# Performance work log

Measured on AMD Instinct MI355X. Metric: run time of the kernel, lower is better.

The kernel has to match this reference:

```python
import jax, jax.numpy as jnp
import numpy as np

C = 16          # n_tasks (channels) = num_tasks - 1
NUM_TASKS = 17  # IndexKernel size
RANK = 3        # IndexKernel rank (hard-coded in source)
JITTER = 1e-4
N_MC = 10
N_CLASSES = 10

def _rbf(x1, x2, ls):
    d = (x1[:, None] - x2[None, :]) / ls
    return jnp.exp(-0.5 * d * d)

def _gp_posterior(x, i_tr, y, xs, i_te, c, ls, noise, Btask):
    # Exact GP posterior with Hadamard multitask kernel k(x,x')*B[i,i'].
    T = x.shape[0]
    Kxx = _rbf(x, x, ls) * Btask[i_tr][:, i_tr] + (noise * noise + JITTER) * jnp.eye(T, dtype=x.dtype)
    Ksx = _rbf(xs, x, ls) * Btask[i_te][:, i_tr]
    Kss = _rbf(xs, xs, ls) * Btask[i_te][:, i_te]
    L = jnp.linalg.cholesky(Kxx)
    alpha = jax.scipy.linalg.cho_solve((L, True), y - c)
    mean = c + Ksx @ alpha
    V = jax.scipy.linalg.solve_triangular(L, Ksx.T, lower=True)  # [T, Ts]
    cov = Kss - V.T @ V
    return mean, cov

def _channel_reshape(Z_raw, test_idx):
    # Vectorized version of the triple-loop ragged scatter.
    # Z_raw: [S, B, Ts]; test_idx: [B, Ts] int -> Z: [S, B, max_len, C]
    S, Bb, Ts = Z_raw.shape
    max_len = Ts // C
    onehot = jax.nn.one_hot(test_idx, C, dtype=jnp.int32)                       # [B, Ts, C]
    before = jnp.cumsum(onehot, axis=1) - onehot                                # same-channel count before elem
    pos = jnp.take_along_axis(before, test_idx[..., None], axis=-1)[..., 0]     # [B, Ts]
    b_idx = jnp.broadcast_to(jnp.arange(Bb)[:, None], (Bb, Ts))
    Z = jnp.zeros((S, Bb, max_len, C), Z_raw.dtype)
    return Z.at[:, b_idx, pos, test_idx].set(Z_raw)

def setup_inputs() -> dict:
    key = jax.random.key(0)
    ks = jax.random.split(key, 8)
    B, T, Ts = 32, 1024, 1024
    inputs = jax.random.uniform(ks[0], (B, T, 1), jnp.float32) * 10.0
    indices = jax.random.randint(ks[1], (B, T, 1), 0, C)
    values = jax.random.normal(ks[2], (B, T), jnp.float32)
    test_inputs = jax.random.uniform(ks[3], (B, Ts, 1), jnp.float32) * 10.0
    test_indices = (jnp.arange(Ts, dtype=jnp.int32)[None, :, None] % C) * jnp.ones((B, 1, 1), jnp.int32)
    eps = jax.random.normal(ks[4], (N_MC, B, Ts), jnp.float32)
    mean_const = jnp.zeros((), jnp.float32)
    lengthscale = jnp.ones((), jnp.float32)
    noise = 0.3 * jnp.ones((), jnp.float32)
    W_task = jax.random.normal(ks[5], (NUM_TASKS, RANK), jnp.float32) * 0.3
    v_task = jax.random.uniform(ks[6], (NUM_TASKS,), jnp.float32)
    W_clf = jax.random.normal(ks[7], (C, N_CLASSES), jnp.float32) * 0.1
    b_clf = jnp.zeros((N_CLASSES,), jnp.float32)
    return dict(inputs=inputs, values=values, test_inputs=test_inputs, eps=eps,
                mean_const=mean_const, lengthscale=lengthscale, noise=noise,
                W_task=W_task, v_task=v_task, W_clf=W_clf, b_clf=b_clf,
                indices=indices, test_indices=test_indices)

def reference(inputs, values, test_inputs, eps, mean_const, lengthscale, noise,
              W_task, v_task, W_clf, b_clf, indices, test_indices):
    Btask = W_task @ W_task.T + jnp.diag(jax.nn.softplus(v_task))  # IndexKernel: B = W W^T + diag(v)
    x, xs = inputs[..., 0], test_inputs[..., 0]
    i_tr, i_te = indices[..., 0], test_indices[..., 0]
    mean, cov = jax.vmap(_gp_posterior, in_axes=(0, 0, 0, 0, 0, None, None, None, None))(
        x, i_tr, values, xs, i_te, mean_const, lengthscale, noise, Btask)
    Ts = xs.shape[1]
    Lstar = jnp.linalg.cholesky(cov + JITTER * jnp.eye(Ts, dtype=cov.dtype))
    samples = mean[None] + jnp.einsum('bij,sbj->sbi', Lstar, eps)   # rsample: [S, B, Ts]
    Z = _channel_reshape(samples, i_te)                              # [S, B, max_len, C]
    S, Bb, ml, _ = Z.shape
    Zc = Z.reshape(S * Bb, ml, C)                                    # monte_carlo collapse (flatten(0,1))
    feat = Zc.mean(axis=1)                                           # clf: mean pool + linear
    return feat @ W_clf + b_clf
```

## Files before the change

### kernel.cpp

```cpp
#include <hip/hip_runtime.h>
#include <math.h>

#define TT 1024
#define CH 16
#define SMC 10
#define NCLS 10
#define JIT 1e-4f

__device__ __forceinline__ void tri_map(int tau, int& ti, int& tj) {
    int i = 0, r = tau;
    while (r >= i + 1) { r -= i + 1; i++; }
    ti = i; tj = r;
}

__global__ __launch_bounds__(256) void k_btask(const float* __restrict__ W,
                                               const float* __restrict__ v,
                                               float* __restrict__ Bt) {
    int t = threadIdx.x;
    for (int e = t; e < 17 * 17; e += 256) {
        int i = e / 17, j = e % 17;
        float s = 0.f;
        for (int r = 0; r < 3; r++) s += W[i * 3 + r] * W[j * 3 + r];
        if (i == j) s += log1pf(expf(v[i]));
        Bt[e] = s;
    }
}

__global__ __launch_bounds__(256) void k_build_kxx(const float* __restrict__ x,
                                                   const int* __restrict__ itr,
                                                   const float* __restrict__ lsp,
                                                   const float* __restrict__ noisep,
                                                   const float* __restrict__ Bt,
                                                   float* __restrict__ A, int b0) {
    int bi = blockIdx.x, bj = blockIdx.y, bz = blockIdx.z;
    if (bj > bi) return;
    int b = b0 + bz;
    __shared__ float sxi[128], sxj[128], Btl[289];
    __shared__ int sii[128], sij[128];
    int t = threadIdx.x;
    if (t < 128) { sxi[t] = x[b * TT + bi * 128 + t]; sii[t] = itr[b * TT + bi * 128 + t]; }
    else { int u = t - 128; sxj[u] = x[b * TT + bj * 128 + u]; sij[u] = itr[b * TT + bj * 128 + u]; }
    for (int e = t; e < 289; e += 256) Btl[e] = Bt[e];
    __syncthreads();
    float invls = 1.0f / lsp[0];
    float n2 = noisep[0] * noisep[0] + JIT;
    float* Ab = A + (size_t)bz * TT * TT;
    for (int l = 0; l < 64; l++) {
        int e = l * 256 + t;
        int r = e >> 7, c = e & 127;
        float d = (sxi[r] - sxj[c]) * invls;
        float kv = expf(-0.5f * d * d) * Btl[sii[r] * 17 + sij[c]];
        int gi = bi * 128 + r, gj = bj * 128 + c;
        if (gi == gj) kv += n2;
        Ab[(size_t)gi * TT + gj] = kv;
    }
}

__global__ __launch_bounds__(256) void k_build_g(const float* __restrict__ xs,
                                                 const float* __restrict__ x,
                                                 const int* __restrict__ ite,
                                                 const int* __restrict__ itr,
                                                 const float* __restrict__ lsp,
                                                 const float* __restrict__ Bt,
                                                 float* __restrict__ G, int b0) {
    int bj = blockIdx.x, bi = blockIdx.y, bz = blockIdx.z;
    int b = b0 + bz;
    __shared__ float sxr[128], sxc[128], Btl[289];
    __shared__ int sir[128], sic[128];
    int t = threadIdx.x;
    if (t < 128) { sxr[t] = x[b * TT + bj * 128 + t]; sir[t] = itr[b * TT + bj * 128 + t]; }
    else { int u = t - 128; sxc[u] = xs[b * TT + bi * 128 + u]; sic[u] = ite[b * TT + bi * 128 + u]; }
    for (int e = t; e < 289; e += 256) Btl[e] = Bt[e];
    __syncthreads();
    float invls = 1.0f / lsp[0];
    float* Gb = G + (size_t)bz * TT * TT;
    for (int l = 0; l < 64; l++) {
        int e = l * 256 + t;
        int r = e >> 7, c = e & 127;
        float d = (sxc[c] - sxr[r]) * invls;
        float kv = expf(-0.5f * d * d) * Btl[sic[c] * 17 + sir[r]];
        Gb[(size_t)(bj * 128 + r) * TT + bi * 128 + c] = kv;
    }
}

__global__ __launch_bounds__(256) void k_zinit(const float* __restrict__ values,
                                               const float* __restrict__ mc,
                                               float* __restrict__ zb, int b0) {
    int bz = blockIdx.x, t = threadIdx.x;
    float c0 = mc[0];
    for (int i = t; i < TT; i += 256) zb[bz * TT + i] = values[(size_t)(b0 + bz) * TT + i] - c0;
}

__global__ __launch_bounds__(256) void k_stepA64(float* __restrict__ A,
                                                 float* __restrict__ G,
                                                 float* __restrict__ zb,
                                                 float* __restrict__ Dfac,
                                                 int k, int m, int withG) {
    int bx = blockIdx.x, bz = blockIdx.y;
    float* Ab = A + (size_t)bz * TT * TT;
    float* Gb = G + (size_t)bz * TT * TT;
    int kb = k * 64;
    __shared__ float Ld[64][65];
    __shared__ float WK[64][129];
    __shared__ float invl[64];
    __shared__ float zs[64];
    int t = threadIdx.x;
    for (int l = 0; l < 16; l++) {
        int e = l * 256 + t; int r = e >> 6, c = e & 63;
        Ld[r][c] = Ab[(size_t)(kb + r) * TT + kb + c];
    }
    int jtype = 0, r0 = 0, c0 = 0;
    if (bx >= 1 && bx <= m) {
        jtype = 1; r0 = kb + 64 * bx;
        for (int l = 0; l < 16; l++) {
            int e = l * 256 + t; int r = e >> 6, c = e & 63;
            WK[r][c] = Ab[(size_t)(r0 + r) * TT + kb + c];
        }
    } else if (withG && bx >= m + 1 && bx <= m + 8) {
        jtype = 2; c0 = (bx - m - 1) * 128;
        for (int l = 0; l < 32; l++) {
            int e = l * 256 + t; int r = e >> 7, c = e & 127;
            WK[r][c] = Gb[(size_t)(kb + r) * TT + c0 + c];
        }
    } else if (withG && bx == m + 9) {
        jtype = 3;
        if (t < 64) zs[t] = zb[bz * TT + kb + t];
    }
    __syncthreads();
    for (int j = 0; j < 64; j++) {
        if (t == j) { float d = sqrtf(Ld[j][j]); Ld[j][j] = d; invl[j] = 1.0f / d; }
        __syncthreads();
        float lij = 0.f;
        if (t < 64 && t > j) { lij = Ld[t][j] * invl[j]; Ld[t][j] = lij; }
        __syncthreads();
        if (t < 64 && t > j) {
#pragma unroll 4
            for (int p = j + 1; p <= t; p++) Ld[t][p] -= lij * Ld[p][j];
        }
    }
    __syncthreads();
    if (jtype == 0) {
        if (bx == 0) {
            float* Df = Dfac + ((size_t)bz * 16 + k) * 4096;
            for (int l = 0; l < 16; l++) {
                int e = l * 256 + t; int r = e >> 6, c = e & 63;
                Df[r * 64 + c] = Ld[r][c];
            }
        }
        return;
    }
    if (jtype == 1) {
        if (t < 64) {
            for (int j = 0; j < 64; j++) {
                float xv = WK[t][j] * invl[j];
                WK[t][j] = xv;
#pragma unroll 4
                for (int p = j + 1; p < 64; p++) WK[t][p] -= Ld[p][j] * xv;
            }
        }
        __syncthreads();
        for (int l = 0; l < 16; l++) {
            int e = l * 256 + t; int r = e >> 6, c = e & 63;
            Ab[(size_t)(r0 + r) * TT + kb + c] = WK[r][c];
        }
    } else if (jtype == 2) {
        if (t < 128) {
            for (int j = 0; j < 64; j++) {
                float xv = WK[j][t] * invl[j];
                WK[j][t] = xv;
#pragma unroll 4
                for (int p = j + 1; p < 64; p++) WK[p][t] -= Ld[p][j] * xv;
            }
        }
        __syncthreads();
        for (int l = 0; l < 32; l++) {
            int e = l * 256 + t; int r = e >> 7, c = e & 127;
            Gb[(size_t)(kb + r) * TT + c0 + c] = WK[r][c];
        }
    } else {
        if (t == 0) {
            for (int j = 0; j < 64; j++) {
                float zv = zs[j] * invl[j];
                zs[j] = zv;
#pragma unroll 4
                for (int p = j + 1; p < 64; p++) zs[p] -= Ld[p][j] * zv;
            }
        }
        __syncthreads();
        if (t < 64) zb[bz * TT + kb + t] = zs[t];
    }
}

__global__ __launch_bounds__(256) void k_diagfix64(float* __restrict__ A,
                                                   const float* __restrict__ Dfac) {
    int k = blockIdx.x, bz = blockIdx.y;
    int kb = k * 64;
    float* Ab = A + (size_t)bz * TT * TT;
    const float* Df = Dfac + ((size_t)bz * 16 + k) * 4096;
    int t = threadIdx.x;
    for (int l = 0; l < 16; l++) {
        int e = l * 256 + t; int r = e >> 6, c = e & 63;
        if (c <= r) Ab[(size_t)(kb + r) * TT + kb + c] = Df[r * 64 + c];
    }
}

__global__ __launch_bounds__(256) void k_stepB64(float* __restrict__ A,
                                                 float* __restrict__ G,
                                                 float* __restrict__ zb,
                                                 int k, int m, int bc, int withG) {
    int lin = blockIdx.x;
    int slot = lin & 7, q = lin >> 3;
    int beta = ((slot - 4 * (q & 1)) & 7) + (blockIdx.y << 3);
    if (beta >= bc) return;
    float* Ab = A + (size_t)beta * TT * TT;
    float* Gb = G + (size_t)beta * TT * TT;
    int kb = k * 64;
    int nt = (64 * m + 127) / 128;
    int TL = nt * (nt + 1) / 2;
    __shared__ __align__(16) float At[32][132];
    __shared__ __align__(16) float Bs[32][132];
    __shared__ float zk[64];
    int t = threadIdx.x, tx = t & 15, ty = t >> 4;
    if (q < TL) {
        int ti, tj; tri_map(q, ti, tj);
        int base = kb + 64;
        int r0 = base + ti * 128, c0 = base + tj * 128;
        int rvi = TT - r0; if (rvi > 128) rvi = 128;
        int rvj = TT - c0; if (rvj > 128) rvj = 128;
        float acc[8][8] = {};
        for (int s = 0; s < 2; s++) {
            int k0 = kb + s * 32;
            __syncthreads();
            for (int l = 0; l < 4; l++) {
                int f = l * 256 + t;
                int r = f >> 3, c4 = (f & 7) * 4;
                float4 va = make_float4(0.f, 0.f, 0.f, 0.f), vb = make_float4(0.f, 0.f, 0.f, 0.f);
                if (r < rvi) va = *reinterpret_cast<const float4*>(&Ab[(size_t)(r0 + r) * TT + k0 + c4]);
                if (r < rvj) vb = *reinterpret_cast<const float4*>(&Ab[(size_t)(c0 + r) * TT + k0 + c4]);
                At[c4 + 0][r] = va.x; At[c4 + 1][r] = va.y; At[c4 + 2][r] = va.z; At[c4 + 3][r] = va.w;
                Bs[c4 + 0][r] = vb.x; Bs[c4 + 1][r] = vb.y; Bs[c4 + 2][r] = vb.z; Bs[c4 + 3][r] = vb.w;
            }
            __syncthreads();
#pragma unroll 4
            for (int p = 0; p < 32; p++) {
                float4 a0 = *reinterpret_cast<const float4*>(&At[p][ty * 8]);
                float4 a1 = *reinterpret_cast<const float4*>(&At[p][ty * 8 + 4]);
                float4 b0 = *reinterpret_cast<const float4*>(&Bs[p][tx * 4]);
                float4 b1 = *reinterpret_cast<const float4*>(&Bs[p][tx * 4 + 64]);
                float aa[8] = {a0.x, a0.y, a0.z, a0.w, a1.x, a1.y, a1.z, a1.w};
                float bl[4] = {b0.x, b0.y, b0.z, b0.w};
                float bh[4] = {b1.x, b1.y, b1.z, b1.w};
                for (int i = 0; i < 8; i++) {
                    for (int j = 0; j < 4; j++) acc[i][j] += aa[i] * bl[j];
                    for (int j = 0; j < 4; j++) acc[i][j + 4] += aa[i] * bh[j];
                }
            }
        }
        if (tx * 4 >= rvj) return;
        for (int i = 0; i < 8; i++) {
            int rr = ty * 8 + i;
            if (rr >= rvi) break;
            float* cp0 = &Ab[(size_t)(r0 + rr) * TT + c0 + tx * 4];
            float4 cv0 = *reinterpret_cast<float4*>(cp0);
            cv0.x -= acc[i][0]; cv0.y -= acc[i][1]; cv0.z -= acc[i][2]; cv0.w -= acc[i][3];
            *reinterpret_cast<float4*>(cp0) = cv0;
            if (rvj > 64) {
                float* cp1 = cp0 + 64;
                float4 cv1 = *reinterpret_cast<float4*>(cp1);
                cv1.x -= acc[i][4]; cv1.y -= acc[i][5]; cv1.z -= acc[i][6]; cv1.w -= acc[i][7];
                *reinterpret_cast<float4*>(cp1) = cv1;
            }
        }
        return;
    }
    int e = q - TL;
    int ti = e / 9, sub = e % 9;
    int r0 = kb + 64 + ti * 128;
    int rvi = TT - r0; if (rvi > 128) rvi = 128;
    if (sub < 8) {
        int c0 = sub * 128;
        float acc[8][8] = {};
        for (int s = 0; s < 2; s++) {
            int k0 = kb + s * 32;
            __syncthreads();
            for (int l = 0; l < 4; l++) {
                int f = l * 256 + t;
                int r = f >> 3, c4 = (f & 7) * 4;
                float4 va = make_float4(0.f, 0.f, 0.f, 0.f);
                if (r < rvi) va = *reinterpret_cast<const float4*>(&Ab[(size_t)(r0 + r) * TT + k0 + c4]);
                At[c4 + 0][r] = va.x; At[c4 + 1][r] = va.y; At[c4 + 2][r] = va.z; At[c4 + 3][r] = va.w;
                int kr = f >> 5, cc4 = (f & 31) * 4;
                float4 vb = *reinterpret_cast<const float4*>(&Gb[(size_t)(k0 + kr) * TT + c0 + cc4]);
                *reinterpret_cast<float4*>(&Bs[kr][cc4]) = vb;
            }
            __syncthreads();
#pragma unroll 4
            for (int p = 0; p < 32; p++) {
                float4 a0 = *reinterpret_cast<const float4*>(&At[p][ty * 8]);
                float4 a1 = *reinterpret_cast<const float4*>(&At[p][ty * 8 + 4]);
                float4 b0 = *reinterpret_cast<const float4*>(&Bs[p][tx * 4]);
                float4 b1 = *reinterpret_cast<const float4*>(&Bs[p][tx * 4 + 64]);
                float aa[8] = {a0.x, a0.y, a0.z, a0.w, a1.x, a1.y, a1.z, a1.w};
                float bl[4] = {b0.x, b0.y, b0.z, b0.w};
                float bh[4] = {b1.x, b1.y, b1.z, b1.w};
                for (int i = 0; i < 8; i++) {
                    for (int j = 0; j < 4; j++) acc[i][j] += aa[i] * bl[j];
                    for (int j = 0; j < 4; j++) acc[i][j + 4] += aa[i] * bh[j];
                }
            }
        }
        for (int i = 0; i < 8; i++) {
            int rr = ty * 8 + i;
            if (rr >= rvi) break;
            float* cp0 = &Gb[(size_t)(r0 + rr) * TT + c0 + tx * 4];
            float4 cv0 = *reinterpret_cast<float4*>(cp0);
            cv0.x -= acc[i][0]; cv0.y -= acc[i][1]; cv0.z -= acc[i][2]; cv0.w -= acc[i][3];
            *reinterpret_cast<float4*>(cp0) = cv0;
            float* cp1 = cp0 + 64;
            float4 cv1 = *reinterpret_cast<float4*>(cp1);
            cv1.x -= acc[i][4]; cv1.y -= acc[i][5]; cv1.z -= acc[i][6]; cv1.w -= acc[i][7];
            *reinterpret_cast<float4*>(cp1) = cv1;
        }
    } else {
        if (t < 64) zk[t] = zb[beta * TT + kb + t];
        float accz = 0.f;
        for (int s = 0; s < 2; s++) {
            int k0 = kb + s * 32;
            __syncthreads();
            for (int l = 0; l < 4; l++) {
                int f = l * 256 + t;
                int r = f >> 3, c4 = (f & 7) * 4;
                float4 va = make_float4(0.f, 0.f, 0.f, 0.f);
                if (r < rvi) va = *reinterpret_cast<const float4*>(&Ab[(size_t)(r0 + r) * TT + k0 + c4]);
                At[c4 + 0][r] = va.x; At[c4 + 1][r] = va.y; At[c4 + 2][r] = va.z; At[c4 + 3][r] = va.w;
            }
            __syncthreads();
            if (t < 128) {
                for (int qq = 0; qq < 32; qq++) accz += At[qq][t] * zk[s * 32 + qq];
            }
        }
        if (t < rvi) zb[beta * TT + r0 + t] -= accz;
    }
}

__global__ __launch_bounds__(256) void k_cov64(const float* __restrict__ G,
                                               const float* __restrict__ xs,
                                               const int* __restrict__ ite,
                                               const float* __restrict__ lsp,
                                               const float* __restrict__ Bt,
                                               float* __restrict__ A,
                                               const float* __restrict__ zb,
                                               const float* __restrict__ mc,
                                               float* __restrict__ meanb,
                                               int b0, int bc) {
    int lin = blockIdx.x;
    int slot = lin & 7, tau = lin >> 3;
    int beta = ((slot - 4 * (tau & 1)) & 7) + (blockIdx.y << 3);
    if (beta >= bc) return;
    int ti, tj; tri_map(tau, ti, tj);
    int b = b0 + beta;
    const float* Gb = G + (size_t)beta * TT * TT;
    float* Ab = A + (size_t)beta * TT * TT;
    int i0 = ti * 64, j0 = tj * 64;
    __shared__ __align__(16) float Va[32][68];
    __shared__ __align__(16) float Vb[32][68];
    __shared__ float sxi[64], sxj[64], Btl[289], zs[32];
    __shared__ int sei[64], sej[64];
    int t = threadIdx.x, tx = t & 15, ty = t >> 4;
    if (t < 64) { sxi[t] = xs[b * TT + i0 + t]; sei[t] = ite[b * TT + i0 + t]; }
    else if (t < 128) { int u = t - 64; sxj[u] = xs[b * TT + j0 + u]; sej[u] = ite[b * TT + j0 + u]; }
    for (int e = t; e < 289; e += 256) Btl[e] = Bt[e];
    bool diag = (ti == tj);
    float acc[4][4] = {};
    float macc[4] = {0.f, 0.f, 0.f, 0.f};
    for (int k0 = 0; k0 < TT; k0 += 32) {
        __syncthreads();
        for (int l = 0; l < 2; l++) {
            int f = l * 256 + t;
            int kr = f >> 4, cc4 = (f & 15) * 4;
            *reinterpret_cast<float4*>(&Va[kr][cc4]) =
                *reinterpret_cast<const float4*>(&Gb[(size_t)(k0 + kr) * TT + i0 + cc4]);
            *reinterpret_cast<float4*>(&Vb[kr][cc4]) =
                *reinterpret_cast<const float4*>(&Gb[(size_t)(k0 + kr) * TT + j0 + cc4]);
        }
        if (diag && t < 32) zs[t] = zb[beta * TT + k0 + t];
        __syncthreads();
#pragma unroll 4
        for (int p = 0; p < 32; p++) {
            float4 av = *reinterpret_cast<const float4*>(&Va[p][ty * 4]);
            float4 bv = *reinterpret_cast<const float4*>(&Vb[p][tx * 4]);
            float aa[4] = {av.x, av.y, av.z, av.w};
            float bb[4] = {bv.x, bv.y, bv.z, bv.w};
            for (int i = 0; i < 4; i++)
                for (int j = 0; j < 4; j++) acc[i][j] += aa[i] * bb[j];
        }
        if (diag && ty == 0) {
#pragma unroll 4
            for (int p = 0; p < 32; p++) {
                float zv = zs[p];
                float4 av = *reinterpret_cast<const float4*>(&Va[p][tx * 4]);
                macc[0] += av.x * zv; macc[1] += av.y * zv;
                macc[2] += av.z * zv; macc[3] += av.w * zv;
            }
        }
    }
    float invls = 1.0f / lsp[0];
    for (int i = 0; i < 4; i++) {
        int ri = ty * 4 + i; int gi = i0 + ri;
        float xi = sxi[ri]; int ci = sei[ri] * 17;
        float vo[4];
        for (int j = 0; j < 4; j++) {
            int rj = tx * 4 + j; int gj = j0 + rj;
            float d = (xi - sxj[rj]) * invls;
            float v = expf(-0.5f * d * d) * Btl[ci + sej[rj]] - acc[i][j];
            if (gi == gj) v += JIT;
            vo[j] = v;
        }
        *reinterpret_cast<float4*>(&Ab[(size_t)gi * TT + j0 + tx * 4]) =
            make_float4(vo[0], vo[1], vo[2], vo[3]);
    }
    if (diag && ty == 0) {
        float c0 = mc[0];
        for (int j = 0; j < 4; j++)
            meanb[(size_t)b * TT + i0 + tx * 4 + j] = c0 + macc[j];
    }
}

__global__ __launch_bounds__(256) void k_P(const float* __restrict__ A,
                                           const int* __restrict__ ite,
                                           float* __restrict__ P, int b0) {
    int bz = blockIdx.y; int b = b0 + bz;
    const float* Ab = A + (size_t)bz * TT * TT;
    __shared__ int chl[TT];
    __shared__ float accl[CH * 256];
    int t = threadIdx.x;
    for (int i = t; i < TT; i += 256) chl[i] = ite[b * TT + i];
    for (int c = 0; c < CH; c++) accl[c * 256 + t] = 0.f;
    __syncthreads();
    int j0 = blockIdx.x * 256;
    int j = j0 + t;
    for (int i = j0; i < TT; i++) {
        float v = Ab[(size_t)i * TT + j];
        if (i >= j) accl[chl[i] * 256 + t] += v;
    }
    for (int c = 0; c < CH; c++) P[((size_t)b * CH + c) * TT + j] = accl[c * 256 + t];
}

__global__ __launch_bounds__(64) void k_msum(const float* __restrict__ meanb,
                                             const int* __restrict__ ite,
                                             float* __restrict__ msum, int b0) {
    int bz = blockIdx.x; int b = b0 + bz;
    __shared__ float pacc[CH][65];
    int t = threadIdx.x;
    for (int c = 0; c < CH; c++) pacc[c][t] = 0.f;
    __syncthreads();
    for (int i = t; i < TT; i += 64) pacc[ite[b * TT + i]][t] += meanb[b * TT + i];
    __syncthreads();
    if (t < CH) {
        float s = 0.f;
        for (int u = 0; u < 64; u++) s += pacc[t][u];
        msum[b * CH + t] = s;
    }
}

__global__ __launch_bounds__(256) void k_featout(const float* __restrict__ P,
                                                 const float* __restrict__ msum,
                                                 const float* __restrict__ eps,
                                                 const float* __restrict__ Wc,
                                                 const float* __restrict__ bc_,
                                                 float* __restrict__ out, int b0, int Btot) {
    int s = blockIdx.x; int b = b0 + blockIdx.y;
    __shared__ float el[TT];
    __shared__ float part[256];
    __shared__ float featl[CH];
    int t = threadIdx.x;
    for (int i = t; i < TT; i += 256) el[i] = eps[((size_t)s * Btot + b) * TT + i];
    __syncthreads();
    int c = t >> 4, seg = t & 15;
    float acc = 0.f;
    const float* Pr = &P[((size_t)b * CH + c) * TT + seg * 64];
    for (int j = 0; j < 64; j++) acc += Pr[j] * el[seg * 64 + j];
    part[t] = acc;
    __syncthreads();
    if (t < CH) {
        float s2 = msum[b * CH + t];
        for (int g = 0; g < 16; g++) s2 += part[t * 16 + g];
        featl[t] = s2 * (1.0f / 64.0f);
    }
    __syncthreads();
    if (t < NCLS) {
        float o = bc_[t];
        for (int c2 = 0; c2 < CH; c2++) o += featl[c2] * Wc[c2 * NCLS + t];
        out[((size_t)s * Btot + b) * NCLS + t] = o;
    }
}

extern "C" void kernel_launch(void* const* d_in, const int* in_sizes, int n_in,
                              void* d_out, int out_size, void* d_ws, size_t ws_size,
                              hipStream_t stream) {
    const float* inputs       = (const float*)d_in[0];
    const float* values       = (const float*)d_in[1];
    const float* test_inputs  = (const float*)d_in[2];
    const float* eps          = (const float*)d_in[3];
    const float* mc           = (const float*)d_in[4];
    const float* ls           = (const float*)d_in[5];
    const float* noise        = (const float*)d_in[6];
    const float* W_task       = (const float*)d_in[7];
    const float* v_task       = (const float*)d_in[8];
    const float* W_clf        = (const float*)d_in[9];
    const float* b_clf        = (const float*)d_in[10];
    const int*   indices      = (const int*)d_in[11];
    const int*   test_indices = (const int*)d_in[12];
    float* out = (float*)d_out;

    int Btot = in_sizes[1] / TT;

    float* ws = (float*)d_ws;
    size_t off = 0;
    float* Bt    = ws + off; off += 512;
    float* zbuf  = ws + off; off += (size_t)Btot * TT;
    float* meanb = ws + off; off += (size_t)Btot * TT;
    float* Pb    = ws + off; off += (size_t)Btot * CH * TT;
    float* msum  = ws + off; off += (size_t)Btot * CH;
    off = (off + 63) & ~(size_t)63;

    size_t avail = (ws_size / 4 > off) ? (ws_size / 4 - off) : 0;
    size_t per = 2 * (size_t)TT * TT + 16 * 4096;
    int chunk = (int)(avail / per);
    if (chunk < 1) chunk = 1;
    if (chunk > Btot) chunk = Btot;
    float* bigA = ws + off;
    float* bigG = bigA + (size_t)chunk * TT * TT;
    float* Dfac = bigG + (size_t)chunk * TT * TT;

    k_btask<<<1, 256, 0, stream>>>(W_task, v_task, Bt);

    for (int b0 = 0; b0 < Btot; b0 += chunk) {
        int bcc = chunk; if (b0 + bcc > Btot) bcc = Btot - b0;
        int by = (bcc + 7) / 8;

        k_build_kxx<<<dim3(8, 8, bcc), 256, 0, stream>>>(inputs, indices, ls, noise, Bt, bigA, b0);
        k_build_g<<<dim3(8, 8, bcc), 256, 0, stream>>>(test_inputs, inputs, test_indices, indices, ls, Bt, bigG, b0);
        k_zinit<<<bcc, 256, 0, stream>>>(values, mc, zbuf, b0);
        for (int k = 0; k < 16; k++) {
            int m = 15 - k;
            k_stepA64<<<dim3(m + 10, bcc), 256, 0, stream>>>(bigA, bigG, zbuf, Dfac, k, m, 1);
            int nt = (64 * m + 127) / 128;
            int Q = nt * (nt + 1) / 2 + nt * 9;
            if (m > 0) k_stepB64<<<dim3(Q * 8, by), 256, 0, stream>>>(bigA, bigG, zbuf, k, m, bcc, 1);
        }
        k_cov64<<<dim3(136 * 8, by), 256, 0, stream>>>(bigG, test_inputs, test_indices, ls, Bt,
                                                       bigA, zbuf, mc, meanb, b0, bcc);
        for (int k = 0; k < 16; k++) {
            int m = 15 - k;
            k_stepA64<<<dim3(m + 1, bcc), 256, 0, stream>>>(bigA, bigA, zbuf, Dfac, k, m, 0);
            int nt = (64 * m + 127) / 128;
            int Q = nt * (nt + 1) / 2;
            if (m > 0) k_stepB64<<<dim3(Q * 8, by), 256, 0, stream>>>(bigA, bigA, zbuf, k, m, bcc, 0);
        }
        k_diagfix64<<<dim3(16, bcc), 256, 0, stream>>>(bigA, Dfac);
        k_P<<<dim3(4, bcc), 256, 0, stream>>>(bigA, test_indices, Pb, b0);
        k_msum<<<bcc, 64, 0, stream>>>(meanb, test_indices, msum, b0);
        k_featout<<<dim3(SMC, bcc), 256, 0, stream>>>(Pb, msum, eps, W_clf, b_clf, out, b0, Btot);
    }
}
```

Baseline: 10.14 ms.

## Move diagonal block factorization out of per-block solve into trailing update kernel

Before, every block of the panel-solve kernel redundantly Cholesky-factored the 64x64 diagonal block before doing its triangular solve. Now a separate kernel factors the first diagonal block, and the trailing-update kernel gets one extra block that applies the rank-64 update to the next diagonal block, factors it and stores it in Dfac. The solve kernel then just loads the precomputed factor. This removes the serial 64-step factorization from every solve block's critical path, at the cost of a serial factorization block inside the update launch and a special case that skips writing the next diagonal block.

Result: faster. 9.590 ms (-5.4%).

```diff
diff --git a/kernel.cpp b/kernel.cpp
--- a/kernel.cpp
+++ b/kernel.cpp
@@ -91,11 +91,42 @@
     for (int i = t; i < TT; i += 256) zb[bz * TT + i] = values[(size_t)(b0 + bz) * TT + i] - c0;
 }
 
-__global__ __launch_bounds__(256) void k_stepA64(float* __restrict__ A,
-                                                 float* __restrict__ G,
-                                                 float* __restrict__ zb,
-                                                 float* __restrict__ Dfac,
-                                                 int k, int m, int withG) {
+__global__ __launch_bounds__(256) void k_factor0(const float* __restrict__ A,
+                                                 float* __restrict__ Dfac) {
+    int bz = blockIdx.x;
+    const float* Ab = A + (size_t)bz * TT * TT;
+    __shared__ float Ld[64][65];
+    __shared__ float invl[64];
+    int t = threadIdx.x;
+    for (int l = 0; l < 16; l++) {
+        int e = l * 256 + t; int r = e >> 6, c = e & 63;
+        Ld[r][c] = Ab[(size_t)r * TT + c];
+    }
+    __syncthreads();
+    for (int j = 0; j < 64; j++) {
+        if (t == j) { float d = sqrtf(Ld[j][j]); Ld[j][j] = d; invl[j] = 1.0f / d; }
+        __syncthreads();
+        float lij = 0.f;
+        if (t < 64 && t > j) { lij = Ld[t][j] * invl[j]; Ld[t][j] = lij; }
+        __syncthreads();
+        if (t < 64 && t > j) {
+#pragma unroll 4
+            for (int p = j + 1; p <= t; p++) Ld[t][p] -= lij * Ld[p][j];
+        }
+    }
+    __syncthreads();
+    float* Df = Dfac + (size_t)bz * 16 * 4096;
+    for (int l = 0; l < 16; l++) {
+        int e = l * 256 + t; int r = e >> 6, c = e & 63;
+        Df[r * 64 + c] = Ld[r][c];
+    }
+}
+
+__global__ __launch_bounds__(256) void k_solveA(float* __restrict__ A,
+                                                float* __restrict__ G,
+                                                float* __restrict__ zb,
+                                                const float* __restrict__ Dfac,
+                                                int k, int m, int withG) {
     int bx = blockIdx.x, bz = blockIdx.y;
     float* Ab = A + (size_t)bz * TT * TT;
     float* Gb = G + (size_t)bz * TT * TT;
@@ -105,50 +136,31 @@
     __shared__ float invl[64];
     __shared__ float zs[64];
     int t = threadIdx.x;
+    const float* Df = Dfac + ((size_t)bz * 16 + k) * 4096;
     for (int l = 0; l < 16; l++) {
         int e = l * 256 + t; int r = e >> 6, c = e & 63;
-        Ld[r][c] = Ab[(size_t)(kb + r) * TT + kb + c];
-    }
-    int jtype = 0, r0 = 0, c0 = 0;
-    if (bx >= 1 && bx <= m) {
-        jtype = 1; r0 = kb + 64 * bx;
+        Ld[r][c] = Df[r * 64 + c];
+    }
+    int jtype, r0 = 0, c0 = 0;
+    if (bx < m) {
+        jtype = 1; r0 = kb + 64 * (bx + 1);
         for (int l = 0; l < 16; l++) {
             int e = l * 256 + t; int r = e >> 6, c = e & 63;
             WK[r][c] = Ab[(size_t)(r0 + r) * TT + kb + c];
         }
-    } else if (withG && bx >= m + 1 && bx <= m + 8) {
-        jtype = 2; c0 = (bx - m - 1) * 128;
+    } else if (withG && bx < m + 8) {
+        jtype = 2; c0 = (bx - m) * 128;
         for (int l = 0; l < 32; l++) {
             int e = l * 256 + t; int r = e >> 7, c = e & 127;
             WK[r][c] = Gb[(size_t)(kb + r) * TT + c0 + c];
         }
-    } else if (withG && bx == m + 9) {
+    } else {
         jtype = 3;
         if (t < 64) zs[t] = zb[bz * TT + kb + t];
     }
     __syncthreads();
-    for (int j = 0; j < 64; j++) {
-        if (t == j) { float d = sqrtf(Ld[j][j]); Ld[j][j] = d; invl[j] = 1.0f / d; }
-        __syncthreads();
-        float lij = 0.f;
-        if (t < 64 && t > j) { lij = Ld[t][j] * invl[j]; Ld[t][j] = lij; }
-        __syncthreads();
-        if (t < 64 && t > j) {
-#pragma unroll 4
-            for (int p = j + 1; p <= t; p++) Ld[t][p] -= lij * Ld[p][j];
-        }
-    }
-    __syncthreads();
-    if (jtype == 0) {
-        if (bx == 0) {
-            float* Df = Dfac + ((size_t)bz * 16 + k) * 4096;
-            for (int l = 0; l < 16; l++) {
-                int e = l * 256 + t; int r = e >> 6, c = e & 63;
-                Df[r * 64 + c] = Ld[r][c];
-            }
-        }
-        return;
-    }
+    if (t < 64) invl[t] = 1.0f / Ld[t][t];
+    __syncthreads();
     if (jtype == 1) {
         if (t < 64) {
             for (int j = 0; j < 64; j++) {
@@ -207,6 +219,7 @@
 __global__ __launch_bounds__(256) void k_stepB64(float* __restrict__ A,
                                                  float* __restrict__ G,
                                                  float* __restrict__ zb,
+                                                 float* __restrict__ Dfac,
                                                  int k, int m, int bc, int withG) {
     int lin = blockIdx.x;
     int slot = lin & 7, q = lin >> 3;
@@ -217,9 +230,14 @@
     int kb = k * 64;
     int nt = (64 * m + 127) / 128;
     int TL = nt * (nt + 1) / 2;
-    __shared__ __align__(16) float At[32][132];
-    __shared__ __align__(16) float Bs[32][132];
+    int gz = withG ? 9 * nt : 0;
+    __shared__ __align__(16) float sm[8448];
+    float (*At)[132] = reinterpret_cast<float (*)[132]>(sm);
+    float (*Bs)[132] = reinterpret_cast<float (*)[132]>(sm + 4224);
+    float (*FLd)[65] = reinterpret_cast<float (*)[65]>(sm);
+    float (*FPn)[65] = reinterpret_cast<float (*)[65]>(sm + 4160);
     __shared__ float zk[64];
+    __shared__ float finv[64];
     int t = threadIdx.x, tx = t & 15, ty = t >> 4;
     if (q < TL) {
         int ti, tj; tri_map(q, ti, tj);
@@ -260,86 +278,134 @@
         for (int i = 0; i < 8; i++) {
             int rr = ty * 8 + i;
             if (rr >= rvi) break;
-            float* cp0 = &Ab[(size_t)(r0 + rr) * TT + c0 + tx * 4];
-            float4 cv0 = *reinterpret_cast<float4*>(cp0);
-            cv0.x -= acc[i][0]; cv0.y -= acc[i][1]; cv0.z -= acc[i][2]; cv0.w -= acc[i][3];
-            *reinterpret_cast<float4*>(cp0) = cv0;
+            if (!(q == 0 && rr < 64)) {
+                float* cp0 = &Ab[(size_t)(r0 + rr) * TT + c0 + tx * 4];
+                float4 cv0 = *reinterpret_cast<float4*>(cp0);
+                cv0.x -= acc[i][0]; cv0.y -= acc[i][1]; cv0.z -= acc[i][2]; cv0.w -= acc[i][3];
+                *reinterpret_cast<float4*>(cp0) = cv0;
+            }
             if (rvj > 64) {
+                float* cp1 = &Ab[(size_t)(r0 + rr) * TT + c0 + 64 + tx * 4];
+                float4 cv1 = *reinterpret_cast<float4*>(cp1);
+                cv1.x -= acc[i][4]; cv1.y -= acc[i][5]; cv1.z -= acc[i][6]; cv1.w -= acc[i][7];
+                *reinterpret_cast<float4*>(cp1) = cv1;
+            }
+        }
+        return;
+    }
+    if (q < TL + gz) {
+        int e = q - TL;
+        int ti = e / 9, sub = e % 9;
+        int r0 = kb + 64 + ti * 128;
+        int rvi = TT - r0; if (rvi > 128) rvi = 128;
+        if (sub < 8) {
+            int c0 = sub * 128;
+            float acc[8][8] = {};
+            for (int s = 0; s < 2; s++) {
+                int k0 = kb + s * 32;
+                __syncthreads();
+                for (int l = 0; l < 4; l++) {
+                    int f = l * 256 + t;
+                    int r = f >> 3, c4 = (f & 7) * 4;
+                    float4 va = make_float4(0.f, 0.f, 0.f, 0.f);
+                    if (r < rvi) va = *reinterpret_cast<const float4*>(&Ab[(size_t)(r0 + r) * TT + k0 + c4]);
+                    At[c4 + 0][r] = va.x; At[c4 + 1][r] = va.y; At[c4 + 2][r] = va.z; At[c4 + 3][r] = va.w;
+                    int kr = f >> 5, cc4 = (f & 31) * 4;
+                    float4 vb = *reinterpret_cast<const float4*>(&Gb[(size_t)(k0 + kr) * TT + c0 + cc4]);
+                    *reinterpret_cast<float4*>(&Bs[kr][cc4]) = vb;
+                }
+                __syncthreads();
+#pragma unroll 4
+                for (int p = 0; p < 32; p++) {
+                    float4 a0 = *reinterpret_cast<const float4*>(&At[p][ty * 8]);
+                    float4 a1 = *reinterpret_cast<const float4*>(&At[p][ty * 8 + 4]);
+                    float4 b0 = *reinterpret_cast<const float4*>(&Bs[p][tx * 4]);
+                    float4 b1 = *reinterpret_cast<const float4*>(&Bs[p][tx * 4 + 64]);
+                    float aa[8] = {a0.x, a0.y, a0.z, a0.w, a1.x, a1.y, a1.z, a1.w};
+                    float bl[4] = {b0.x, b0.y, b0.z, b0.w};
+                    float bh[4] = {b1.x, b1.y, b1.z, b1.w};
+                    for (int i = 0; i < 8; i++) {
+                        for (int j = 0; j < 4; j++) acc[i][j] += aa[i] * bl[j];
+                        for (int j = 0; j < 4; j++) acc[i][j + 4] += aa[i] * bh[j];
+                    }
+                }
+            }
+            for (int i = 0; i < 8; i++) {
+                int rr = ty * 8 + i;
+                if (rr >= rvi) break;
+                float* cp0 = &Gb[(size_t)(r0 + rr) * TT + c0 + tx * 4];
+                float4 cv0 = *reinterpret_cast<float4*>(cp0);
+                cv0.x -= acc[i][0]; cv0.y -= acc[i][1]; cv0.z -= acc[i][2]; cv0.w -= acc[i][3];
+                *reinterpret_cast<float4*>(cp0) = cv0;
                 float* cp1 = cp0 + 64;
                 float4 cv1 = *reinterpret_cast<float4*>(cp1);
                 cv1.x -= acc[i][4]; cv1.y -= acc[i][5]; cv1.z -= acc[i][6]; cv1.w -= acc[i][7];
                 *reinterpret_cast<float4*>(cp1) = cv1;
             }
+        } else {
+            if (t < 64) zk[t] = zb[beta * TT + kb + t];
+            float accz = 0.f;
+            for (int s = 0; s < 2; s++) {
+                int k0 = kb + s * 32;
+                __syncthreads();
+                for (int l = 0; l < 4; l++) {
+                    int f = l * 256 + t;
+                    int r = f >> 3, c4 = (f & 7) * 4;
+                    float4 va = make_float4(0.f, 0.f, 0.f, 0.f);
+                    if (r < rvi) va = *reinterpret_cast<const float4*>(&Ab[(size_t)(r0 + r) * TT + k0 + c4]);
+                    At[c4 + 0][r] = va.x; At[c4 + 1][r] = va.y; At[c4 + 2][r] = va.z; At[c4 + 3][r] = va.w;
+                }
+                __syncthreads();
+                if (t < 128) {
+                    for (int qq = 0; qq < 32; qq++) accz += At[qq][t] * zk[s * 32 + qq];
+                }
+            }
+            if (t < rvi) zb[beta * TT + r0 + t] -= accz;
         }
         return;
     }
-    int e = q - TL;
-    int ti = e / 9, sub = e % 9;
-    int r0 = kb + 64 + ti * 128;
-    int rvi = TT - r0; if (rvi > 128) rvi = 128;
-    if (sub < 8) {
-        int c0 = sub * 128;
-        float acc[8][8] = {};
-        for (int s = 0; s < 2; s++) {
-            int k0 = kb + s * 32;
+    {
+        int kb2 = kb + 64;
+        for (int l = 0; l < 16; l++) {
+            int e = l * 256 + t; int r = e >> 6, c = e & 63;
+            FLd[r][c] = Ab[(size_t)(kb2 + r) * TT + kb2 + c];
+            FPn[r][c] = Ab[(size_t)(kb2 + r) * TT + kb + c];
+        }
+        __syncthreads();
+        {
+            float acc[4][4] = {};
+            for (int p = 0; p < 64; p++) {
+                float a0 = FPn[ty * 4 + 0][p], a1 = FPn[ty * 4 + 1][p];
+                float a2 = FPn[ty * 4 + 2][p], a3 = FPn[ty * 4 + 3][p];
+                float b0 = FPn[tx * 4 + 0][p], b1 = FPn[tx * 4 + 1][p];
+                float b2 = FPn[tx * 4 + 2][p], b3 = FPn[tx * 4 + 3][p];
+                acc[0][0] += a0 * b0; acc[0][1] += a0 * b1; acc[0][2] += a0 * b2; acc[0][3] += a0 * b3;
+                acc[1][0] += a1 * b0; acc[1][1] += a1 * b1; acc[1][2] += a1 * b2; acc[1][3] += a1 * b3;
+                acc[2][0] += a2 * b0; acc[2][1] += a2 * b1; acc[2][2] += a2 * b2; acc[2][3] += a2 * b3;
+                acc[3][0] += a3 * b0; acc[3][1] += a3 * b1; acc[3][2] += a3 * b2; acc[3][3] += a3 * b3;
+            }
+            for (int i = 0; i < 4; i++)
+                for (int j = 0; j < 4; j++)
+                    FLd[ty * 4 + i][tx * 4 + j] -= acc[i][j];
+        }
+        __syncthreads();
+        for (int j = 0; j < 64; j++) {
+            if (t == j) { float d = sqrtf(FLd[j][j]); FLd[j][j] = d; finv[j] = 1.0f / d; }
             __syncthreads();
-            for (int l = 0; l < 4; l++) {
-                int f = l * 256 + t;
-                int r = f >> 3, c4 = (f & 7) * 4;
-                float4 va = make_float4(0.f, 0.f, 0.f, 0.f);
-                if (r < rvi) va = *reinterpret_cast<const float4*>(&Ab[(size_t)(r0 + r) * TT + k0 + c4]);
-                At[c4 + 0][r] = va.x; At[c4 + 1][r] = va.y; At[c4 + 2][r] = va.z; At[c4 + 3][r] = va.w;
-                int kr = f >> 5, cc4 = (f & 31) * 4;
-                float4 vb = *reinterpret_cast<const float4*>(&Gb[(size_t)(k0 + kr) * TT + c0 + cc4]);
-                *reinterpret_cast<float4*>(&Bs[kr][cc4]) = vb;
-            }
+            float lij = 0.f;
+            if (t < 64 && t > j) { lij = FLd[t][j] * finv[j]; FLd[t][j] = lij; }
             __syncthreads();
-#pragma unroll 4
-            for (int p = 0; p < 32; p++) {
-                float4 a0 = *reinterpret_cast<const float4*>(&At[p][ty * 8]);
-                float4 a1 = *reinterpret_cast<const float4*>(&At[p][ty * 8 + 4]);
-                float4 b0 = *reinterpret_cast<const float4*>(&Bs[p][tx * 4]);
-                float4 b1 = *reinterpret_cast<const float4*>(&Bs[p][tx * 4 + 64]);
-                float aa[8] = {a0.x, a0.y, a0.z, a0.w, a1.x, a1.y, a1.z, a1.w};
-                float bl[4] = {b0.x, b0.y, b0.z, b0.w};
-                float bh[4] = {b1.x, b1.y, b1.z, b1.w};
-                for (int i = 0; i < 8; i++) {
-                    for (int j = 0; j < 4; j++) acc[i][j] += aa[i] * bl[j];
-                    for (int j = 0; j < 4; j++) acc[i][j + 4] += aa[i] * bh[j];
-                }
-            }
-        }
-        for (int i = 0; i < 8; i++) {
-            int rr = ty * 8 + i;
-            if (rr >= rvi) break;
-            float* cp0 = &Gb[(size_t)(r0 + rr) * TT + c0 + tx * 4];
-            float4 cv0 = *reinterpret_cast<float4*>(cp0);
-            cv0.x -= acc[i][0]; cv0.y -= acc[i][1]; cv0.z -= acc[i][2]; cv0.w -= acc[i][3];
-            *reinterpret_cast<float4*>(cp0) = cv0;
-            float* cp1 = cp0 + 64;
-            float4 cv1 = *reinterpret_cast<float4*>(cp1);
-            cv1.x -= acc[i][4]; cv1.y -= acc[i][5]; cv1.z -= acc[i][6]; cv1.w -= acc[i][7];
-            *reinterpret_cast<float4*>(cp1) = cv1;
-        }
-    } else {
-        if (t < 64) zk[t] = zb[beta * TT + kb + t];
-        float accz = 0.f;
-        for (int s = 0; s < 2; s++) {
-            int k0 = kb + s * 32;
-            __syncthreads();
-            for (int l = 0; l < 4; l++) {
-                int f = l * 256 + t;
-                int r = f >> 3, c4 = (f & 7) * 4;
-                float4 va = make_float4(0.f, 0.f, 0.f, 0.f);
-                if (r < rvi) va = *reinterpret_cast<const float4*>(&Ab[(size_t)(r0 + r) * TT + k0 + c4]);
-                At[c4 + 0][r] = va.x; At[c4 + 1][r] = va.y; At[c4 + 2][r] = va.z; At[c4 + 3][r] = va.w;
-            }
-            __syncthreads();
-            if (t < 128) {
-                for (int qq = 0; qq < 32; qq++) accz += At[qq][t] * zk[s * 32 + qq];
-            }
-        }
-        if (t < rvi) zb[beta * TT + r0 + t] -= accz;
+            if (t < 64 && t > j) {
+#pragma unroll 4
+                for (int p = j + 1; p <= t; p++) FLd[t][p] -= lij * FLd[p][j];
+            }
+        }
+        __syncthreads();
+        float* DfO = Dfac + ((size_t)beta * 16 + (k + 1)) * 4096;
+        for (int l = 0; l < 16; l++) {
+            int e = l * 256 + t; int r = e >> 6, c = e & 63;
+            DfO[r * 64 + c] = FLd[r][c];
+        }
     }
 }
 
@@ -542,21 +608,27 @@
         k_build_kxx<<<dim3(8, 8, bcc), 256, 0, stream>>>(inputs, indices, ls, noise, Bt, bigA, b0);
         k_build_g<<<dim3(8, 8, bcc), 256, 0, stream>>>(test_inputs, inputs, test_indices, indices, ls, Bt, bigG, b0);
         k_zinit<<<bcc, 256, 0, stream>>>(values, mc, zbuf, b0);
+        k_factor0<<<bcc, 256, 0, stream>>>(bigA, Dfac);
         for (int k = 0; k < 16; k++) {
             int m = 15 - k;
-            k_stepA64<<<dim3(m + 10, bcc), 256, 0, stream>>>(bigA, bigG, zbuf, Dfac, k, m, 1);
-            int nt = (64 * m + 127) / 128;
-            int Q = nt * (nt + 1) / 2 + nt * 9;
-            if (m > 0) k_stepB64<<<dim3(Q * 8, by), 256, 0, stream>>>(bigA, bigG, zbuf, k, m, bcc, 1);
+            k_solveA<<<dim3(m + 9, bcc), 256, 0, stream>>>(bigA, bigG, zbuf, Dfac, k, m, 1);
+            if (m > 0) {
+                int nt = (64 * m + 127) / 128;
+                int nq = nt * (nt + 1) / 2 + 9 * nt + 1;
+                k_stepB64<<<dim3(nq * 8, by), 256, 0, stream>>>(bigA, bigG, zbuf, Dfac, k, m, bcc, 1);
+            }
         }
         k_cov64<<<dim3(136 * 8, by), 256, 0, stream>>>(bigG, test_inputs, test_indices, ls, Bt,
                                                        bigA, zbuf, mc, meanb, b0, bcc);
+        k_factor0<<<bcc, 256, 0, stream>>>(bigA, Dfac);
         for (int k = 0; k < 16; k++) {
             int m = 15 - k;
-            k_stepA64<<<dim3(m + 1, bcc), 256, 0, stream>>>(bigA, bigA, zbuf, Dfac, k, m, 0);
-            int nt = (64 * m + 127) / 128;
-            int Q = nt * (nt + 1) / 2;
-            if (m > 0) k_stepB64<<<dim3(Q * 8, by), 256, 0, stream>>>(bigA, bigA, zbuf, k, m, bcc, 0);
+            if (m > 0) {
+                k_solveA<<<dim3(m, bcc), 256, 0, stream>>>(bigA, bigA, zbuf, Dfac, k, m, 0);
+                int nt = (64 * m + 127) / 128;
+                int nq = nt * (nt + 1) / 2 + 1;
+                k_stepB64<<<dim3(nq * 8, by), 256, 0, stream>>>(bigA, bigA, zbuf, Dfac, k, m, bcc, 0);
+            }
         }
         k_diagfix64<<<dim3(16, bcc), 256, 0, stream>>>(bigA, Dfac);
         k_P<<<dim3(4, bcc), 256, 0, stream>>>(bigA, test_indices, Pb, b0);
```
